# Kernel optimization log

Measured on AMD Instinct MI355X. Metric: run time of the kernel, lower is better.

The kernel has to match this reference:

```python
import jax, jax.numpy as jnp
import numpy as np

IN_FEATURES = 11008
OUT_FEATURES = 4096
TOPK = 5504            # in_features * topk_ratio (0.5)
RECALL_THRES = 0.9
N_CACHE = 64           # modeled steady-state cache size


def setup_inputs() -> dict:
    key = jax.random.key(0)
    k1, k2, k3, k4 = jax.random.split(key, 4)
    x = jax.random.normal(k1, (1, 1, IN_FEATURES), dtype=jnp.float32)
    weight = jax.random.normal(k2, (OUT_FEATURES, IN_FEATURES), dtype=jnp.float32) * 0.02
    bias = jax.random.normal(k3, (OUT_FEATURES,), dtype=jnp.float32) * 0.02
    cached_indices = jax.random.randint(k4, (N_CACHE, TOPK), 0, IN_FEATURES, dtype=jnp.int64)
    return {"x": x, "weight": weight, "bias": bias, "cached_indices": cached_indices}


def reference(x, weight, bias, cached_indices):
    # decode path: bsz == seq == 1
    xf = x.reshape(-1, IN_FEATURES)                       # [1, in]
    x_mean = jnp.abs(xf).mean(axis=0)                     # [in]
    # top-k neuron selection (argsort descending -> top_k)
    _, topk_idx = jax.lax.top_k(x_mean, TOPK)             # [topk]
    topk_mask = jnp.zeros((IN_FEATURES,), dtype=bool).at[topk_idx].set(True)
    # rebuild cached boolean masks from cached index sets
    cached_masks = (
        jnp.zeros((N_CACHE, IN_FEATURES), dtype=bool)
        .at[jnp.arange(N_CACHE)[:, None], cached_indices]
        .set(True)
    )
    # recall of each cached mask against current top-k mask
    intersection = jnp.sum(cached_masks & topk_mask[None, :], axis=1)  # [n_cache]
    recalls = intersection.astype(jnp.float32) / TOPK
    best_idx = jnp.argmax(recalls)
    best_recall = recalls[best_idx]
    # cache hit -> reuse cached indices; miss -> use fresh top-k indices
    idx = jnp.where(best_recall >= RECALL_THRES, cached_indices[best_idx], topk_idx)
    # gather sparse column slice, then small GEMM + bias
    w_slice = weight[:, idx]                               # [out, topk]
    out = xf[:, idx] @ w_slice.T + bias                    # [1, out]
    return out.reshape(1, 1, OUT_FEATURES)
```

## Files before the change

kernel.cpp:

```cpp
#include <hip/hip_runtime.h>
#include <stdint.h>

#define IN_F   11008
#define OUT_F  4096
#define TOPK_K 5504
#define NCACHE 64
#define MASK_WORDS 344
#define NCHUNK 11
#define ROWS_PER_BLOCK 16
#define GEMV_THREADS   512


__device__ __forceinline__ unsigned absbits(float v) {
    return __float_as_uint(v) & 0x7fffffffu;
}

__global__ __launch_bounds__(1024) void k_select_prefetch(const float* __restrict__ x,
                                                          const float* __restrict__ W,
                                                          unsigned* __restrict__ maskbits_g,
                                                          unsigned* __restrict__ flag_g) {
    __shared__ unsigned hist[16][256];
    __shared__ unsigned csum[256];
    __shared__ unsigned sh_T, sh_rem, sh_totEq;
    __shared__ unsigned waveEq[NCHUNK][16];
    __shared__ unsigned waveEqPre[NCHUNK][16];

    const int tid  = threadIdx.x;
    const int wv   = tid >> 6;
    const int lane = tid & 63;
    const int bid  = blockIdx.x;

    if (bid != 0) {
        const float4* wp = (const float4*)(W + (size_t)bid * (ROWS_PER_BLOCK * IN_F));
        const int NCH = (ROWS_PER_BLOCK * IN_F / 4) / (2 * 1024);
        for (int c = 0; c < NCH; ++c) {
            if (c >= 1 && __hip_atomic_load(flag_g, __ATOMIC_RELAXED, __HIP_MEMORY_SCOPE_AGENT) != 0u)
                break;
            float4 a = wp[c * 2048 + tid];
            float4 b = wp[c * 2048 + 1024 + tid];
            asm volatile("" :: "v"(a.x), "v"(a.y), "v"(a.z), "v"(a.w));
            asm volatile("" :: "v"(b.x), "v"(b.y), "v"(b.z), "v"(b.w));
        }
        return;
    }

    const int nk = (tid < IN_F - 10 * 1024) ? NCHUNK : NCHUNK - 1;

    unsigned key[NCHUNK];
#pragma unroll
    for (int c = 0; c < NCHUNK; ++c) {
        key[c] = 0u;
        if (c < nk) key[c] = absbits(x[c * 1024 + tid]);
    }

    unsigned prefix = 0, maskHi = 0, remaining = TOPK_K;

    for (int pass = 3; pass >= 0; --pass) {
        const int sh = pass * 8;
        for (int b = tid; b < 16 * 256; b += 1024) ((unsigned*)hist)[b] = 0;
        __syncthreads();
#pragma unroll
        for (int c = 0; c < NCHUNK; ++c) {
            if (c < nk && (key[c] & maskHi) == prefix)
                atomicAdd(&hist[wv][(key[c] >> sh) & 255], 1u);
        }
        __syncthreads();
        if (tid < 256) {
            unsigned s = 0;
#pragma unroll
            for (int w = 0; w < 16; ++w) s += hist[w][tid];
            csum[tid] = s;
        }
        __syncthreads();
        if (wv == 0) {
            unsigned c0 = csum[4 * lane + 0], c1 = csum[4 * lane + 1];
            unsigned c2 = csum[4 * lane + 2], c3 = csum[4 * lane + 3];
            unsigned S = c0 + c1 + c2 + c3;
#pragma unroll
            for (int off = 1; off < 64; off <<= 1) {
                unsigned v = __shfl_down(S, off, 64);
                if (lane + off < 64) S += v;
            }
            unsigned Sn = __shfl_down(S, 1, 64);
            if (lane == 63) Sn = 0;
            unsigned t3 = Sn + c3;
            unsigned t2 = t3 + c2;
            unsigned t1 = t2 + c1;
            unsigned t0 = t1 + c0;
            unsigned rem = remaining;
            if (t3 >= rem && Sn < rem) { sh_T = prefix | ((unsigned)(4 * lane + 3) << sh); sh_rem = rem - Sn; }
            if (t2 >= rem && t3 < rem) { sh_T = prefix | ((unsigned)(4 * lane + 2) << sh); sh_rem = rem - t3; }
            if (t1 >= rem && t2 < rem) { sh_T = prefix | ((unsigned)(4 * lane + 1) << sh); sh_rem = rem - t2; }
            if (t0 >= rem && t1 < rem) { sh_T = prefix | ((unsigned)(4 * lane + 0) << sh); sh_rem = rem - t1; }
        }
        __syncthreads();
        prefix = sh_T;
        maskHi |= 0xffu << sh;
        remaining = sh_rem;
    }

    const unsigned T = prefix;
    const unsigned eqTake = remaining;

    unsigned gtm = 0, eqm = 0;
#pragma unroll
    for (int c = 0; c < NCHUNK; ++c) {
        if (c < nk) {
            if (key[c] > T)       gtm |= 1u << c;
            else if (key[c] == T) eqm |= 1u << c;
        }
    }
#pragma unroll
    for (int c = 0; c < NCHUNK; ++c) {
        unsigned long long bal = __ballot((eqm >> c) & 1u);
        if (lane == 0) waveEq[c][wv] = (unsigned)__popcll(bal);
    }
    __syncthreads();
    if (tid < 64) {
        unsigned s = 0;
        for (int p = lane; p < NCHUNK * 16; p += 64) s += waveEq[p >> 4][p & 15];
#pragma unroll
        for (int off = 32; off > 0; off >>= 1) s += __shfl_down(s, off, 64);
        if (lane == 0) sh_totEq = s;
    }
    __syncthreads();
    const bool fast = (sh_totEq == eqTake);
    if (!fast) {
        if (tid == 0) {
            unsigned run = 0;
            for (int c = 0; c < NCHUNK; ++c)
                for (int w = 0; w < 16; ++w) { waveEqPre[c][w] = run; run += waveEq[c][w]; }
        }
        __syncthreads();
    }
#pragma unroll
    for (int c = 0; c < NCHUNK; ++c) {
        bool eq = (eqm >> c) & 1u;
        bool take;
        if (fast) {
            take = (((gtm >> c) & 1u) != 0u) || eq;
        } else {
            unsigned long long balEq = __ballot(eq);
            unsigned rank = waveEqPre[c][wv] + (unsigned)__popcll(balEq & ((1ull << lane) - 1ull));
            take = (((gtm >> c) & 1u) != 0u) || (eq && rank < eqTake);
        }
        unsigned long long balT = __ballot(take);
        int w0 = c * 32 + wv * 2;
        if (w0 < MASK_WORDS && lane == 0) {
            maskbits_g[w0]     = (unsigned)balT;
            maskbits_g[w0 + 1] = (unsigned)(balT >> 32);
        }
    }
    __syncthreads();
    if (tid == 0)
        __hip_atomic_store(flag_g, 1u, __ATOMIC_RELAXED, __HIP_MEMORY_SCOPE_AGENT);
}

__global__ __launch_bounds__(GEMV_THREADS) void k_recall_gemv(const float* __restrict__ x,
                                                              const float* __restrict__ W,
                                                              const float* __restrict__ bias,
                                                              const int* __restrict__ cached,
                                                              const unsigned* __restrict__ maskbits_g,
                                                              unsigned* __restrict__ score_g,
                                                              unsigned* __restrict__ done_g,
                                                              float* __restrict__ out) {
    __shared__ __align__(16) float xs[IN_F];
    __shared__ unsigned rowbits[MASK_WORDS];
    __shared__ unsigned wsum[8];
    const int tid  = threadIdx.x;
    const int wv   = tid >> 6;
    const int lane = tid & 63;
    const int bid  = blockIdx.x;

    if (bid < NCACHE) {
        for (int w = tid; w < MASK_WORDS; w += GEMV_THREADS) rowbits[w] = 0;
        __syncthreads();
        const int4* ci4 = (const int4*)(cached + (size_t)bid * TOPK_K);
        for (int t = tid; t < TOPK_K / 4; t += GEMV_THREADS) {
            int4 v = ci4[t];
            atomicOr(&rowbits[v.x >> 5], 1u << (v.x & 31));
            atomicOr(&rowbits[v.y >> 5], 1u << (v.y & 31));
            atomicOr(&rowbits[v.z >> 5], 1u << (v.z & 31));
            atomicOr(&rowbits[v.w >> 5], 1u << (v.w & 31));
        }
        __syncthreads();
        unsigned cnt = 0;
        for (int w = tid; w < MASK_WORDS; w += GEMV_THREADS) cnt += __popc(rowbits[w] & maskbits_g[w]);
        for (int off = 32; off > 0; off >>= 1) cnt += __shfl_down(cnt, off, 64);
        if (lane == 0) wsum[wv] = cnt;
        __syncthreads();
        if (tid == 0) {
            unsigned tot = 0;
#pragma unroll
            for (int w = 0; w < 8; ++w) tot += wsum[w];
            atomicMax(score_g, (tot << 6) | (unsigned)(63 - bid));
            __hip_atomic_fetch_add(done_g, 1u, __ATOMIC_RELEASE, __HIP_MEMORY_SCOPE_AGENT);
        }
        return;
    }

    const int g = bid - NCACHE;
    const float4* x4 = (const float4*)x;
    for (int j = tid; j < IN_F / 4; j += GEMV_THREADS) {
        float4 xv = x4[j];
        int base = j * 4;
        unsigned wbits = maskbits_g[base >> 5];
        int sh = base & 31;
        xs[base + 0] = xv.x * (float)((wbits >> (sh + 0)) & 1u);
        xs[base + 1] = xv.y * (float)((wbits >> (sh + 1)) & 1u);
        xs[base + 2] = xv.z * (float)((wbits >> (sh + 2)) & 1u);
        xs[base + 3] = xv.w * (float)((wbits >> (sh + 3)) & 1u);
    }
    __syncthreads();

    const int row0 = g * ROWS_PER_BLOCK + wv * 2;
    const int row1 = row0 + 1;
    const float4* w0p = (const float4*)(W + (size_t)row0 * IN_F);
    const float4* w1p = (const float4*)(W + (size_t)row1 * IN_F);
    const float4* xs4 = (const float4*)xs;

    float acc0 = 0.f, acc1 = 0.f;
#pragma unroll 4
    for (int j = lane; j < IN_F / 4; j += 64) {
        float4 xv = xs4[j];
        float4 a  = w0p[j];
        float4 b  = w1p[j];
        acc0 += xv.x * a.x + xv.y * a.y + xv.z * a.z + xv.w * a.w;
        acc1 += xv.x * b.x + xv.y * b.y + xv.z * b.z + xv.w * b.w;
    }
    for (int off = 32; off > 0; off >>= 1) {
        acc0 += __shfl_down(acc0, off, 64);
        acc1 += __shfl_down(acc1, off, 64);
    }

    if (tid == 0) {
        while (__hip_atomic_load(done_g, __ATOMIC_ACQUIRE, __HIP_MEMORY_SCOPE_AGENT) < NCACHE)
            __builtin_amdgcn_s_sleep(2);
    }
    __syncthreads();

    unsigned score = *score_g;
    bool useCache = ((float)(score >> 6) / (float)TOPK_K) >= 0.9f;
    if (!useCache) {
        if (lane == 0) {
            out[row0] = acc0 + bias[row0];
            out[row1] = acc1 + bias[row1];
        }
    } else {
        int best = 63 - (int)(score & 63u);
        __syncthreads();
        for (int i = tid; i < IN_F; i += GEMV_THREADS) xs[i] = 0.f;
        __syncthreads();
        const int* ci = cached + (size_t)best * TOPK_K;
        for (int t = tid; t < TOPK_K; t += GEMV_THREADS) {
            int idx = ci[t];
            atomicAdd(&xs[idx], x[idx]);
        }
        __syncthreads();
        float a0 = 0.f, a1 = 0.f;
#pragma unroll 4
        for (int j = lane; j < IN_F / 4; j += 64) {
            float4 xv = xs4[j];
            float4 a  = w0p[j];
            float4 b  = w1p[j];
            a0 += xv.x * a.x + xv.y * a.y + xv.z * a.z + xv.w * a.w;
            a1 += xv.x * b.x + xv.y * b.y + xv.z * b.z + xv.w * b.w;
        }
        for (int off = 32; off > 0; off >>= 1) {
            a0 += __shfl_down(a0, off, 64);
            a1 += __shfl_down(a1, off, 64);
        }
        if (lane == 0) {
            out[row0] = a0 + bias[row0];
            out[row1] = a1 + bias[row1];
        }
    }
}

extern "C" void kernel_launch(void* const* d_in, const int* in_sizes, int n_in,
                              void* d_out, int out_size, void* d_ws, size_t ws_size,
                              hipStream_t stream) {
    const float* x      = (const float*)d_in[0];
    const float* W      = (const float*)d_in[1];
    const float* bias   = (const float*)d_in[2];
    const int*   cached = (const int*)d_in[3];
    float* out = (float*)d_out;

    char* ws = (char*)d_ws;
    unsigned* maskbits = (unsigned*)(ws + 0);
    unsigned* score    = (unsigned*)(ws + 1472);
    unsigned* flag     = (unsigned*)(ws + 1476);
    unsigned* done     = (unsigned*)(ws + 1480);

    hipMemsetAsync(ws + 1472, 0, 12, stream);
    k_select_prefetch<<<256, 1024, 0, stream>>>(x, W, maskbits, flag);
    k_recall_gemv<<<NCACHE + OUT_F / ROWS_PER_BLOCK, GEMV_THREADS, 0, stream>>>(
        x, W, bias, cached, maskbits, score, done, out);
}
```

Baseline: 266.6 us.

## Fuse selection, recall and GEMV into one persistent kernel with flag sync

Merges the top-k selection kernel and the recall/GEMV kernel into a single launch. Block 0 computes the radix-select mask with 512 threads, the cache blocks build their masks and then spin on a release flag, and the GEMV blocks prefetch their own weight rows before waiting on the flag. This removes a kernel launch boundary and lets each GEMV block warm the cache with exactly the rows it will later use. In exchange, selection now runs with half the threads, and the design relies on all 321 blocks being co-resident so the spin-waits cannot deadlock.

```diff
diff --git a/kernel.cpp b/kernel.cpp
--- a/kernel.cpp
+++ b/kernel.cpp
@@ -6,177 +6,162 @@
 #define TOPK_K 5504
 #define NCACHE 64
 #define MASK_WORDS 344
-#define NCHUNK 11
+#define NTHR   512
+#define NCHUNK 22
 #define ROWS_PER_BLOCK 16
-#define GEMV_THREADS   512
+#define NGEMV  (OUT_F / ROWS_PER_BLOCK)
+#define NBLK   (1 + NCACHE + NGEMV)
 
 
 __device__ __forceinline__ unsigned absbits(float v) {
     return __float_as_uint(v) & 0x7fffffffu;
 }
 
-__global__ __launch_bounds__(1024) void k_select_prefetch(const float* __restrict__ x,
-                                                          const float* __restrict__ W,
-                                                          unsigned* __restrict__ maskbits_g,
-                                                          unsigned* __restrict__ flag_g) {
-    __shared__ unsigned hist[16][256];
+__global__ __launch_bounds__(NTHR, 4) void k_all(const float* __restrict__ x,
+                                                 const float* __restrict__ W,
+                                                 const float* __restrict__ bias,
+                                                 const int* __restrict__ cached,
+                                                 float* __restrict__ out,
+                                                 unsigned* __restrict__ maskbits_g,
+                                                 unsigned* __restrict__ score_g,
+                                                 unsigned* __restrict__ flag_g,
+                                                 unsigned* __restrict__ done_g) {
+    __shared__ unsigned hist[8][256];
     __shared__ unsigned csum[256];
     __shared__ unsigned sh_T, sh_rem, sh_totEq;
-    __shared__ unsigned waveEq[NCHUNK][16];
-    __shared__ unsigned waveEqPre[NCHUNK][16];
+    __shared__ unsigned waveEq[NCHUNK][8];
+    __shared__ unsigned waveEqPre[NCHUNK][8];
+    __shared__ unsigned rowbits[MASK_WORDS];
+    __shared__ unsigned wsum[8];
+    __shared__ __align__(16) float xs[IN_F];
 
     const int tid  = threadIdx.x;
     const int wv   = tid >> 6;
     const int lane = tid & 63;
     const int bid  = blockIdx.x;
 
-    if (bid != 0) {
-        const float4* wp = (const float4*)(W + (size_t)bid * (ROWS_PER_BLOCK * IN_F));
-        const int NCH = (ROWS_PER_BLOCK * IN_F / 4) / (2 * 1024);
-        for (int c = 0; c < NCH; ++c) {
-            if (c >= 1 && __hip_atomic_load(flag_g, __ATOMIC_RELAXED, __HIP_MEMORY_SCOPE_AGENT) != 0u)
-                break;
-            float4 a = wp[c * 2048 + tid];
-            float4 b = wp[c * 2048 + 1024 + tid];
-            asm volatile("" :: "v"(a.x), "v"(a.y), "v"(a.z), "v"(a.w));
-            asm volatile("" :: "v"(b.x), "v"(b.y), "v"(b.z), "v"(b.w));
+    if (bid == 0) {
+        const int nk = (tid < 256) ? NCHUNK : NCHUNK - 1;
+
+        unsigned key[NCHUNK];
+#pragma unroll
+        for (int c = 0; c < NCHUNK; ++c) {
+            key[c] = 0u;
+            if (c < nk) key[c] = absbits(x[c * NTHR + tid]);
+        }
+
+        unsigned prefix = 0, maskHi = 0, remaining = TOPK_K;
+
+        for (int pass = 3; pass >= 0; --pass) {
+            const int sh = pass * 8;
+            for (int b = tid; b < 8 * 256; b += NTHR) ((unsigned*)hist)[b] = 0;
+            __syncthreads();
+#pragma unroll
+            for (int c = 0; c < NCHUNK; ++c) {
+                if (c < nk && (key[c] & maskHi) == prefix)
+                    atomicAdd(&hist[wv][(key[c] >> sh) & 255], 1u);
+            }
+            __syncthreads();
+            if (tid < 256) {
+                unsigned s = 0;
+#pragma unroll
+                for (int w = 0; w < 8; ++w) s += hist[w][tid];
+                csum[tid] = s;
+            }
+            __syncthreads();
+            if (wv == 0) {
+                unsigned c0 = csum[4 * lane + 0], c1 = csum[4 * lane + 1];
+                unsigned c2 = csum[4 * lane + 2], c3 = csum[4 * lane + 3];
+                unsigned S = c0 + c1 + c2 + c3;
+#pragma unroll
+                for (int off = 1; off < 64; off <<= 1) {
+                    unsigned v = __shfl_down(S, off, 64);
+                    if (lane + off < 64) S += v;
+                }
+                unsigned Sn = __shfl_down(S, 1, 64);
+                if (lane == 63) Sn = 0;
+                unsigned t3 = Sn + c3;
+                unsigned t2 = t3 + c2;
+                unsigned t1 = t2 + c1;
+                unsigned t0 = t1 + c0;
+                unsigned rem = remaining;
+                if (t3 >= rem && Sn < rem) { sh_T = prefix | ((unsigned)(4 * lane + 3) << sh); sh_rem = rem - Sn; }
+                if (t2 >= rem && t3 < rem) { sh_T = prefix | ((unsigned)(4 * lane + 2) << sh); sh_rem = rem - t3; }
+                if (t1 >= rem && t2 < rem) { sh_T = prefix | ((unsigned)(4 * lane + 1) << sh); sh_rem = rem - t2; }
+                if (t0 >= rem && t1 < rem) { sh_T = prefix | ((unsigned)(4 * lane + 0) << sh); sh_rem = rem - t1; }
+            }
+            __syncthreads();
+            prefix = sh_T;
+            maskHi |= 0xffu << sh;
+            remaining = sh_rem;
+        }
+
+        const unsigned T = prefix;
+        const unsigned eqTake = remaining;
+
+        unsigned gtm = 0, eqm = 0;
+#pragma unroll
+        for (int c = 0; c < NCHUNK; ++c) {
+            if (c < nk) {
+                if (key[c] > T)       gtm |= 1u << c;
+                else if (key[c] == T) eqm |= 1u << c;
+            }
+        }
+#pragma unroll
+        for (int c = 0; c < NCHUNK; ++c) {
+            unsigned long long bal = __ballot((eqm >> c) & 1u);
+            if (lane == 0) waveEq[c][wv] = (unsigned)__popcll(bal);
+        }
+        __syncthreads();
+        if (tid < 64) {
+            unsigned s = 0;
+            for (int p = lane; p < NCHUNK * 8; p += 64) s += waveEq[p >> 3][p & 7];
+#pragma unroll
+            for (int off = 32; off > 0; off >>= 1) s += __shfl_down(s, off, 64);
+            if (lane == 0) sh_totEq = s;
+        }
+        __syncthreads();
+        const bool fast = (sh_totEq == eqTake);
+        if (!fast) {
+            if (tid == 0) {
+                unsigned run = 0;
+                for (int c = 0; c < NCHUNK; ++c)
+                    for (int w = 0; w < 8; ++w) { waveEqPre[c][w] = run; run += waveEq[c][w]; }
+            }
+            __syncthreads();
+        }
+#pragma unroll
+        for (int c = 0; c < NCHUNK; ++c) {
+            bool eq = (eqm >> c) & 1u;
+            bool take;
+            if (fast) {
+                take = (((gtm >> c) & 1u) != 0u) || eq;
+            } else {
+                unsigned long long balEq = __ballot(eq);
+                unsigned rank = waveEqPre[c][wv] + (unsigned)__popcll(balEq & ((1ull << lane) - 1ull));
+                take = (((gtm >> c) & 1u) != 0u) || (eq && rank < eqTake);
+            }
+            unsigned long long balT = __ballot(take);
+            int w0 = c * 16 + wv * 2;
+            if (w0 < MASK_WORDS && lane == 0) {
+                maskbits_g[w0]     = (unsigned)balT;
+                maskbits_g[w0 + 1] = (unsigned)(balT >> 32);
+            }
+        }
+        __syncthreads();
+        if (tid == 0) {
+            __threadfence();
+            __hip_atomic_store(flag_g, 1u, __ATOMIC_RELEASE, __HIP_MEMORY_SCOPE_AGENT);
         }
         return;
     }
 
-    const int nk = (tid < IN_F - 10 * 1024) ? NCHUNK : NCHUNK - 1;
-
-    unsigned key[NCHUNK];
-#pragma unroll
-    for (int c = 0; c < NCHUNK; ++c) {
-        key[c] = 0u;
-        if (c < nk) key[c] = absbits(x[c * 1024 + tid]);
-    }
-
-    unsigned prefix = 0, maskHi = 0, remaining = TOPK_K;
-
-    for (int pass = 3; pass >= 0; --pass) {
-        const int sh = pass * 8;
-        for (int b = tid; b < 16 * 256; b += 1024) ((unsigned*)hist)[b] = 0;
-        __syncthreads();
-#pragma unroll
-        for (int c = 0; c < NCHUNK; ++c) {
-            if (c < nk && (key[c] & maskHi) == prefix)
-                atomicAdd(&hist[wv][(key[c] >> sh) & 255], 1u);
-        }
-        __syncthreads();
-        if (tid < 256) {
-            unsigned s = 0;
-#pragma unroll
-            for (int w = 0; w < 16; ++w) s += hist[w][tid];
-            csum[tid] = s;
-        }
-        __syncthreads();
-        if (wv == 0) {
-            unsigned c0 = csum[4 * lane + 0], c1 = csum[4 * lane + 1];
-            unsigned c2 = csum[4 * lane + 2], c3 = csum[4 * lane + 3];
-            unsigned S = c0 + c1 + c2 + c3;
-#pragma unroll
-            for (int off = 1; off < 64; off <<= 1) {
-                unsigned v = __shfl_down(S, off, 64);
-                if (lane + off < 64) S += v;
-            }
-            unsigned Sn = __shfl_down(S, 1, 64);
-            if (lane == 63) Sn = 0;
-            unsigned t3 = Sn + c3;
-            unsigned t2 = t3 + c2;
-            unsigned t1 = t2 + c1;
-            unsigned t0 = t1 + c0;
-            unsigned rem = remaining;
-            if (t3 >= rem && Sn < rem) { sh_T = prefix | ((unsigned)(4 * lane + 3) << sh); sh_rem = rem - Sn; }
-            if (t2 >= rem && t3 < rem) { sh_T = prefix | ((unsigned)(4 * lane + 2) << sh); sh_rem = rem - t3; }
-            if (t1 >= rem && t2 < rem) { sh_T = prefix | ((unsigned)(4 * lane + 1) << sh); sh_rem = rem - t2; }
-            if (t0 >= rem && t1 < rem) { sh_T = prefix | ((unsigned)(4 * lane + 0) << sh); sh_rem = rem - t1; }
-        }
-        __syncthreads();
-        prefix = sh_T;
-        maskHi |= 0xffu << sh;
-        remaining = sh_rem;
-    }
-
-    const unsigned T = prefix;
-    const unsigned eqTake = remaining;
-
-    unsigned gtm = 0, eqm = 0;
-#pragma unroll
-    for (int c = 0; c < NCHUNK; ++c) {
-        if (c < nk) {
-            if (key[c] > T)       gtm |= 1u << c;
-            else if (key[c] == T) eqm |= 1u << c;
-        }
-    }
-#pragma unroll
-    for (int c = 0; c < NCHUNK; ++c) {
-        unsigned long long bal = __ballot((eqm >> c) & 1u);
-        if (lane == 0) waveEq[c][wv] = (unsigned)__popcll(bal);
-    }
-    __syncthreads();
-    if (tid < 64) {
-        unsigned s = 0;
-        for (int p = lane; p < NCHUNK * 16; p += 64) s += waveEq[p >> 4][p & 15];
-#pragma unroll
-        for (int off = 32; off > 0; off >>= 1) s += __shfl_down(s, off, 64);
-        if (lane == 0) sh_totEq = s;
-    }
-    __syncthreads();
-    const bool fast = (sh_totEq == eqTake);
-    if (!fast) {
-        if (tid == 0) {
-            unsigned run = 0;
-            for (int c = 0; c < NCHUNK; ++c)
-                for (int w = 0; w < 16; ++w) { waveEqPre[c][w] = run; run += waveEq[c][w]; }
-        }
-        __syncthreads();
-    }
-#pragma unroll
-    for (int c = 0; c < NCHUNK; ++c) {
-        bool eq = (eqm >> c) & 1u;
-        bool take;
-        if (fast) {
-            take = (((gtm >> c) & 1u) != 0u) || eq;
-        } else {
-            unsigned long long balEq = __ballot(eq);
-            unsigned rank = waveEqPre[c][wv] + (unsigned)__popcll(balEq & ((1ull << lane) - 1ull));
-            take = (((gtm >> c) & 1u) != 0u) || (eq && rank < eqTake);
-        }
-        unsigned long long balT = __ballot(take);
-        int w0 = c * 32 + wv * 2;
-        if (w0 < MASK_WORDS && lane == 0) {
-            maskbits_g[w0]     = (unsigned)balT;
-            maskbits_g[w0 + 1] = (unsigned)(balT >> 32);
-        }
-    }
-    __syncthreads();
-    if (tid == 0)
-        __hip_atomic_store(flag_g, 1u, __ATOMIC_RELAXED, __HIP_MEMORY_SCOPE_AGENT);
-}
-
-__global__ __launch_bounds__(GEMV_THREADS) void k_recall_gemv(const float* __restrict__ x,
-                                                              const float* __restrict__ W,
-                                                              const float* __restrict__ bias,
-                                                              const int* __restrict__ cached,
-                                                              const unsigned* __restrict__ maskbits_g,
-                                                              unsigned* __restrict__ score_g,
-                                                              unsigned* __restrict__ done_g,
-                                                              float* __restrict__ out) {
-    __shared__ __align__(16) float xs[IN_F];
-    __shared__ unsigned rowbits[MASK_WORDS];
-    __shared__ unsigned wsum[8];
-    const int tid  = threadIdx.x;
-    const int wv   = tid >> 6;
-    const int lane = tid & 63;
-    const int bid  = blockIdx.x;
-
-    if (bid < NCACHE) {
-        for (int w = tid; w < MASK_WORDS; w += GEMV_THREADS) rowbits[w] = 0;
-        __syncthreads();
-        const int4* ci4 = (const int4*)(cached + (size_t)bid * TOPK_K);
-        for (int t = tid; t < TOPK_K / 4; t += GEMV_THREADS) {
+    if (bid <= NCACHE) {
+        const int r = bid - 1;
+        for (int w = tid; w < MASK_WORDS; w += NTHR) rowbits[w] = 0;
+        __syncthreads();
+        const int4* ci4 = (const int4*)(cached + (size_t)r * TOPK_K);
+        for (int t = tid; t < TOPK_K / 4; t += NTHR) {
             int4 v = ci4[t];
             atomicOr(&rowbits[v.x >> 5], 1u << (v.x & 31));
             atomicOr(&rowbits[v.y >> 5], 1u << (v.y & 31));
@@ -184,8 +169,13 @@
             atomicOr(&rowbits[v.w >> 5], 1u << (v.w & 31));
         }
         __syncthreads();
+        if (tid == 0) {
+            while (__hip_atomic_load(flag_g, __ATOMIC_ACQUIRE, __HIP_MEMORY_SCOPE_AGENT) == 0u)
+                __builtin_amdgcn_s_sleep(8);
+        }
+        __syncthreads();
         unsigned cnt = 0;
-        for (int w = tid; w < MASK_WORDS; w += GEMV_THREADS) cnt += __popc(rowbits[w] & maskbits_g[w]);
+        for (int w = tid; w < MASK_WORDS; w += NTHR) cnt += __popc(rowbits[w] & maskbits_g[w]);
         for (int off = 32; off > 0; off >>= 1) cnt += __shfl_down(cnt, off, 64);
         if (lane == 0) wsum[wv] = cnt;
         __syncthreads();
@@ -193,23 +183,45 @@
             unsigned tot = 0;
 #pragma unroll
             for (int w = 0; w < 8; ++w) tot += wsum[w];
-            atomicMax(score_g, (tot << 6) | (unsigned)(63 - bid));
+            atomicMax(score_g, (tot << 6) | (unsigned)(63 - r));
             __hip_atomic_fetch_add(done_g, 1u, __ATOMIC_RELEASE, __HIP_MEMORY_SCOPE_AGENT);
         }
         return;
     }
 
-    const int g = bid - NCACHE;
-    const float4* x4 = (const float4*)x;
-    for (int j = tid; j < IN_F / 4; j += GEMV_THREADS) {
-        float4 xv = x4[j];
-        int base = j * 4;
-        unsigned wbits = maskbits_g[base >> 5];
-        int sh = base & 31;
-        xs[base + 0] = xv.x * (float)((wbits >> (sh + 0)) & 1u);
-        xs[base + 1] = xv.y * (float)((wbits >> (sh + 1)) & 1u);
-        xs[base + 2] = xv.z * (float)((wbits >> (sh + 2)) & 1u);
-        xs[base + 3] = xv.w * (float)((wbits >> (sh + 3)) & 1u);
+    const int g = bid - 1 - NCACHE;
+    const float4* wp = (const float4*)(W + (size_t)g * (ROWS_PER_BLOCK * IN_F));
+
+    {
+        const int NCH = (ROWS_PER_BLOCK * IN_F / 4) / (2 * NTHR);
+        for (int c = 0; c < NCH; ++c) {
+            if (c >= 1 && __hip_atomic_load(flag_g, __ATOMIC_RELAXED, __HIP_MEMORY_SCOPE_AGENT) != 0u)
+                break;
+            float4 a = wp[c * 2 * NTHR + tid];
+            float4 b = wp[c * 2 * NTHR + NTHR + tid];
+            asm volatile("" :: "v"(a.x), "v"(a.y), "v"(a.z), "v"(a.w));
+            asm volatile("" :: "v"(b.x), "v"(b.y), "v"(b.z), "v"(b.w));
+        }
+    }
+
+    if (tid == 0) {
+        while (__hip_atomic_load(flag_g, __ATOMIC_ACQUIRE, __HIP_MEMORY_SCOPE_AGENT) == 0u)
+            __builtin_amdgcn_s_sleep(8);
+    }
+    __syncthreads();
+
+    {
+        const float4* x4 = (const float4*)x;
+        for (int j = tid; j < IN_F / 4; j += NTHR) {
+            float4 xv = x4[j];
+            int base = j * 4;
+            unsigned wbits = maskbits_g[base >> 5];
+            int sh = base & 31;
+            xs[base + 0] = xv.x * (float)((wbits >> (sh + 0)) & 1u);
+            xs[base + 1] = xv.y * (float)((wbits >> (sh + 1)) & 1u);
+            xs[base + 2] = xv.z * (float)((wbits >> (sh + 2)) & 1u);
+            xs[base + 3] = xv.w * (float)((wbits >> (sh + 3)) & 1u);
+        }
     }
     __syncthreads();
 
@@ -249,10 +261,10 @@
     } else {
         int best = 63 - (int)(score & 63u);
         __syncthreads();
-        for (int i = tid; i < IN_F; i += GEMV_THREADS) xs[i] = 0.f;
+        for (int i = tid; i < IN_F; i += NTHR) xs[i] = 0.f;
         __syncthreads();
         const int* ci = cached + (size_t)best * TOPK_K;
-        for (int t = tid; t < TOPK_K; t += GEMV_THREADS) {
+        for (int t = tid; t < TOPK_K; t += NTHR) {
             int idx = ci[t];
             atomicAdd(&xs[idx], x[idx]);
         }
@@ -293,7 +305,6 @@
     unsigned* done     = (unsigned*)(ws + 1480);
 
     hipMemsetAsync(ws + 1472, 0, 12, stream);
-    k_select_prefetch<<<256, 1024, 0, stream>>>(x, W, maskbits, flag);
-    k_recall_gemv<<<NCACHE + OUT_F / ROWS_PER_BLOCK, GEMV_THREADS, 0, stream>>>(
-        x, W, bias, cached, maskbits, score, done, out);
+    k_all<<<NBLK, NTHR, 0, stream>>>(x, W, bias, cached, out,
+                                     maskbits, score, flag, done);
 }
```

New measurement: 265.5 us. About the same (-0.4%).
